# Optimization experiments

Hardware: AMD Instinct MI355X
Metric: run time of the kernel (lower is better)

The kernel has to match this reference:

```python
import jax, jax.numpy as jnp
import numpy as np
from jax import lax

B, S_IN, T_OUT, H, V = 128, 1024, 128, 512, 32


def gru_cell(x, h, Wih, Whh, bih, bhh):
    # PyTorch GRU cell math: gates ordered (r, z, n)
    gi = x @ Wih.T + bih            # (B, 3H)
    gh = h @ Whh.T + bhh            # (B, 3H)
    ir, iz, inn = jnp.split(gi, 3, axis=-1)
    hr, hz, hn = jnp.split(gh, 3, axis=-1)
    r = jax.nn.sigmoid(ir + hr)
    z = jax.nn.sigmoid(iz + hz)
    n = jnp.tanh(inn + r * hn)
    return (1.0 - z) * n + z * h


def setup_inputs() -> dict:
    key = jax.random.key(0)
    ks = jax.random.split(key, 16)
    s = 0.05
    p = lambda k, shape: (jax.random.normal(k, shape, jnp.float32) * s)
    z = lambda n: jnp.zeros((n,), jnp.float32)
    return {
        "x": jax.random.normal(ks[0], (B, S_IN, 2), jnp.float32),
        "embedding": p(ks[1], (V, H)),
        "enc_Wih0": p(ks[2], (3 * H, 2)), "enc_Whh0": p(ks[3], (3 * H, H)),
        "enc_bih0": z(3 * H), "enc_bhh0": z(3 * H),
        "enc_Wih1": p(ks[4], (3 * H, H)), "enc_Whh1": p(ks[5], (3 * H, H)),
        "enc_bih1": z(3 * H), "enc_bhh1": z(3 * H),
        "dec_Wih0": p(ks[6], (3 * H, H)), "dec_Whh0": p(ks[7], (3 * H, H)),
        "dec_bih0": z(3 * H), "dec_bhh0": z(3 * H),
        "dec_Wih1": p(ks[8], (3 * H, H)), "dec_Whh1": p(ks[9], (3 * H, H)),
        "dec_bih1": z(3 * H), "dec_bhh1": z(3 * H),
        "Wq": p(ks[10], (H, H)), "bq": z(H),
        "Wc": p(ks[11], (V, 2 * H)), "bc": z(V),
    }


def reference(x, embedding,
              enc_Wih0, enc_Whh0, enc_bih0, enc_bhh0,
              enc_Wih1, enc_Whh1, enc_bih1, enc_bhh1,
              dec_Wih0, dec_Whh0, dec_bih0, dec_bhh0,
              dec_Wih1, dec_Whh1, dec_bih1, dec_bhh1,
              Wq, bq, Wc, bc):
    b = x.shape[0]
    h_init = jnp.zeros((b, H), x.dtype)

    def run_layer(xs, Wih, Whh, bih, bhh):
        def step(h, xt):
            h2 = gru_cell(xt, h, Wih, Whh, bih, bhh)
            return h2, h2
        return lax.scan(step, h_init, xs)

    # ----- encoder: 2-layer GRU over time -----
    xs = jnp.swapaxes(x, 0, 1)                       # (S, B, 2)
    hT0, ys0 = run_layer(xs, enc_Wih0, enc_Whh0, enc_bih0, enc_bhh0)
    hT1, ys1 = run_layer(ys0, enc_Wih1, enc_Whh1, enc_bih1, enc_bhh1)
    out_enc = jnp.swapaxes(ys1, 0, 1)                # (B, S, H)

    # ----- greedy decoder with Bahdanau-style dot attention -----
    tok0 = jnp.zeros((b,), jnp.int32)                # start token = 0

    def dec_step(carry, _):
        h0, h1, tok = carry
        emb = embedding[tok]                         # (B, H)
        h0n = gru_cell(emb, h0, dec_Wih0, dec_Whh0, dec_bih0, dec_bhh0)
        h1n = gru_cell(h0n, h1, dec_Wih1, dec_Whh1, dec_bih1, dec_bhh1)
        q = h1n @ Wq.T + bq                          # (B, H)
        att = jnp.einsum('bh,bsh->bs', q, out_enc)   # (B, S)
        w = jax.nn.softmax(att, axis=-1)
        ctx = jnp.einsum('bs,bsh->bh', w, out_enc)   # (B, H)
        logits = jnp.concatenate([h1n, ctx], axis=-1) @ Wc.T + bc  # (B, V)
        tok2 = jnp.argmax(logits, axis=-1).astype(jnp.int32)
        return (h0n, h1n, tok2), (logits, w)

    (h0f, h1f, _), (logits_seq, w_seq) = lax.scan(
        dec_step, (hT0, hT1, tok0), None, length=T_OUT)

    vec_out = jnp.swapaxes(logits_seq, 0, 1)         # (B, T_out, V)
    attn_ws = jnp.transpose(w_seq, (1, 2, 0))        # (B, S, T_out)
    hidden = jnp.stack([h0f, h1f], axis=0)           # (n_layers, B, H)
    return vec_out, hidden, attn_ws
```

## Files before the change

kernel.cpp:

```cpp
#include <hip/hip_runtime.h>
#include <hip/hip_fp16.h>
#include <math.h>

#define HH 512
#define BB 128
#define SS 1024
#define TT 128
#define VV 32
#define GG 1536

__device__ __forceinline__ float sigm(float v){ return 1.f/(1.f+expf(-v)); }
__device__ __forceinline__ float fast_tanh(float x){
  float ax = fabsf(x);
  float t = expf(-2.f*ax);
  float r = (1.f - t)/(1.f + t);
  return copysignf(r, x);
}

struct F8 { float v[8]; };

__device__ __forceinline__ F8 load8(const float* p){
  F8 r;
  float4 a = *reinterpret_cast<const float4*>(p);
  float4 b = *reinterpret_cast<const float4*>(p+4);
  r.v[0]=a.x; r.v[1]=a.y; r.v[2]=a.z; r.v[3]=a.w;
  r.v[4]=b.x; r.v[5]=b.y; r.v[6]=b.z; r.v[7]=b.w;
  return r;
}
__device__ __forceinline__ F8 load8(const __half* p){
  F8 r;
  union { float4 f4; __half2 h2[4]; } u;
  u.f4 = *reinterpret_cast<const float4*>(p);
  #pragma unroll
  for (int i=0;i<4;i++){ float2 f = __half22float2(u.h2[i]); r.v[2*i]=f.x; r.v[2*i+1]=f.y; }
  return r;
}
__device__ __forceinline__ void store_enc(float* p, float v){ *p = v; }
__device__ __forceinline__ void store_enc(__half* p, float v){ *p = __float2half(v); }

__global__ void transpose_k(const float* __restrict__ src, float* __restrict__ dst,
                            int R, int C){
  __shared__ float tile[32][33];
  int c0 = blockIdx.x*32, r0 = blockIdx.y*32;
  int tx = threadIdx.x & 31, ty = threadIdx.x >> 5;
  for (int i = ty; i < 32; i += 8){
    int r = r0 + i, c = c0 + tx;
    tile[i][tx] = (r < R && c < C) ? src[(size_t)r*C + c] : 0.f;
  }
  __syncthreads();
  for (int i = ty; i < 32; i += 8){
    int c = c0 + i, r = r0 + tx;
    if (c < C && r < R) dst[(size_t)c*R + r] = tile[tx][i];
  }
}

__global__ void pack_w(const float* __restrict__ src, float* __restrict__ dst, int R){
  int idx = blockIdx.x*256 + threadIdx.x;
  int r = idx >> 9, k = idx & 511;
  dst[((size_t)(k>>2)*R + r)*4 + (k&3)] = src[idx];
}

__device__ __forceinline__ void dot8(const float4* __restrict__ wp, int row, int NR,
                                     const float4* sh4, float acc[8]){
  float4 wc = wp[row];
  for (int kc = 0; kc < 128; kc++) {
    float4 wn = wp[(size_t)(kc+1)*NR + row];
    #pragma unroll
    for (int i = 0; i < 8; i++) {
      float4 h4 = sh4[i*128 + kc];
      acc[i] = fmaf(wc.w, h4.w, fmaf(wc.z, h4.z, fmaf(wc.y, h4.y, fmaf(wc.x, h4.x, acc[i]))));
    }
    wc = wn;
  }
}

template<typename ET>
__global__ __launch_bounds__(192) void enc_step(
    int p,
    const float* __restrict__ x,
    const float* __restrict__ Wih0,
    const float* __restrict__ bih0, const float* __restrict__ bhh0,
    const float* __restrict__ bih1, const float* __restrict__ bhh1,
    const float* __restrict__ Whh0P, const float* __restrict__ Wih1P,
    const float* __restrict__ Whh1P,
    float* __restrict__ gh_all,
    float* __restrict__ h0buf,
    float* __restrict__ h1buf,
    ET* __restrict__ out_enc)
{
  __shared__ float4 sh4[8*128];
  float* shs = (float*)sh4;
  const int bid = blockIdx.x;
  const int xcd = bid & 7, j = bid >> 3;
  const int rc  = xcd*3 + (j % 3);
  const int bch = j / 3;
  const int m   = rc >> 3;
  const int pb  = p & 1;
  if (m == 0 && p >= SS) return;
  if (m >= 1 && p < 1) return;
  const int b0 = bch*8;
  const int tid = threadIdx.x;

  if (m <= 1) {
    float* h0w = h0buf + (size_t)pb*BB*HH;
    for (int idx = tid; idx < 8*HH; idx += 192) {
      int bl = idx >> 9, e = idx & (HH-1);
      int b = b0 + bl;
      float hv;
      if (p == 0) hv = 0.f;
      else {
        int t0 = p - 1;
        float x0v = x[((size_t)b*SS + t0)*2 + 0];
        float x1v = x[((size_t)b*SS + t0)*2 + 1];
        const float* ghp = gh_all + ((size_t)(1-pb)*3 + 0)*BB*GG + (size_t)b*GG;
        float gir = fmaf(x0v, Wih0[e*2],          fmaf(x1v, Wih0[e*2+1],          bih0[e]));
        float giz = fmaf(x0v, Wih0[(HH+e)*2],     fmaf(x1v, Wih0[(HH+e)*2+1],     bih0[HH+e]));
        float gin = fmaf(x0v, Wih0[(2*HH+e)*2],   fmaf(x1v, Wih0[(2*HH+e)*2+1],   bih0[2*HH+e]));
        float ghr = ghp[e]      + bhh0[e];
        float ghz = ghp[HH+e]   + bhh0[HH+e];
        float ghn = ghp[2*HH+e] + bhh0[2*HH+e];
        float hp = (p == 1) ? 0.f : h0buf[(size_t)(1-pb)*BB*HH + (size_t)b*HH + e];
        float r = sigm(gir + ghr);
        float z = sigm(giz + ghz);
        float n = fast_tanh(fmaf(r, ghn, gin));
        hv = (1.f - z)*n + z*hp;
      }
      h0w[(size_t)b*HH + e] = hv;
      shs[idx] = hv;
    }
  } else {
    float* h1w = h1buf + (size_t)pb*BB*HH;
    for (int idx = tid; idx < 8*HH; idx += 192) {
      int bl = idx >> 9, e = idx & (HH-1);
      int b = b0 + bl;
      float hv;
      if (p <= 1) hv = 0.f;
      else {
        const float* gip = gh_all + ((size_t)(1-pb)*3 + 1)*BB*GG + (size_t)b*GG;
        const float* ghp = gh_all + ((size_t)(1-pb)*3 + 2)*BB*GG + (size_t)b*GG;
        float gir = gip[e]      + bih1[e];
        float giz = gip[HH+e]   + bih1[HH+e];
        float gin = gip[2*HH+e] + bih1[2*HH+e];
        float ghr = ghp[e]      + bhh1[e];
        float ghz = ghp[HH+e]   + bhh1[HH+e];
        float ghn = ghp[2*HH+e] + bhh1[2*HH+e];
        float hp = (p == 2) ? 0.f : h1buf[(size_t)(1-pb)*BB*HH + (size_t)b*HH + e];
        float r = sigm(gir + ghr);
        float z = sigm(giz + ghz);
        float n = fast_tanh(fmaf(r, ghn, gin));
        hv = (1.f - z)*n + z*hp;
      }
      h1w[(size_t)b*HH + e] = hv;
      shs[idx] = hv;
      if (p >= 2) store_enc(out_enc + ((size_t)b*SS + (p-2))*HH + e, hv);
    }
  }
  __syncthreads();

  const float4* WP = (const float4*)((m == 0) ? Whh0P : (m == 1) ? Wih1P : Whh1P);
  const int wv = tid >> 6, lane = tid & 63;
  const int row = (rc & 7)*192 + wv*64 + lane;
  float acc[8] = {0,0,0,0,0,0,0,0};
  dot8(WP, row, GG, sh4, acc);
  float* dst = gh_all + ((size_t)pb*3 + m)*BB*GG;
  #pragma unroll
  for (int i = 0; i < 8; i++) dst[(size_t)(b0+i)*GG + row] = acc[i];
}

template<typename ET>
__global__ void enc_bridge(
    const float* __restrict__ gh_all, const float* __restrict__ h1buf,
    const float* __restrict__ bih1, const float* __restrict__ bhh1,
    float* __restrict__ h1init, ET* __restrict__ out_enc)
{
  int idx = blockIdx.x*256 + threadIdx.x;
  int b = idx >> 9, e = idx & (HH-1);
  const float* gip = gh_all + (size_t)1*BB*GG + (size_t)b*GG;
  const float* ghp = gh_all + (size_t)2*BB*GG + (size_t)b*GG;
  float gir = gip[e]      + bih1[e];
  float giz = gip[HH+e]   + bih1[HH+e];
  float gin = gip[2*HH+e] + bih1[2*HH+e];
  float ghr = ghp[e]      + bhh1[e];
  float ghz = ghp[HH+e]   + bhh1[HH+e];
  float ghn = ghp[2*HH+e] + bhh1[2*HH+e];
  float hp = h1buf[(size_t)b*HH + e];
  float r = sigm(gir + ghr);
  float z = sigm(giz + ghz);
  float n = fast_tanh(fmaf(r, ghn, gin));
  float hv = (1.f - z)*n + z*hp;
  h1init[(size_t)b*HH + e] = hv;
  store_enc(out_enc + ((size_t)b*SS + (SS-1))*HH + e, hv);
}

__global__ __launch_bounds__(192) void dec_step1(
    int t,
    const float* __restrict__ embedding,
    const int* __restrict__ tok,
    const float* __restrict__ bih0d, const float* __restrict__ bhh0d,
    const float* __restrict__ Wih0P, const float* __restrict__ Whh0P,
    const float* __restrict__ h0init,
    float* __restrict__ dgh0,
    float* __restrict__ h0d)
{
  __shared__ float4 sh4[8*128];
  float* shs = (float*)sh4;
  const int bid = blockIdx.x;
  const int xcd = bid & 7, j = bid >> 3;
  const int rc  = xcd*2 + (j & 1);
  const int bch = j >> 1;
  const int m   = rc >> 3;
  const int db  = t & 1;
  const int b0 = bch*8;
  const int tid = threadIdx.x;

  if (m == 1) {
    float* hw = h0d + (size_t)db*BB*HH;
    for (int idx = tid; idx < 8*HH; idx += 192) {
      int bl = idx >> 9, e = idx & (HH-1);
      int b = b0 + bl;
      float hv;
      if (t == 0) hv = h0init[(size_t)b*HH + e];
      else {
        const float* gip = dgh0 + ((size_t)(1-db)*2 + 0)*BB*GG + (size_t)b*GG;
        const float* ghp = dgh0 + ((size_t)(1-db)*2 + 1)*BB*GG + (size_t)b*GG;
        float gir = gip[e]      + bih0d[e];
        float giz = gip[HH+e]   + bih0d[HH+e];
        float gin = gip[2*HH+e] + bih0d[2*HH+e];
        float ghr = ghp[e]      + bhh0d[e];
        float ghz = ghp[HH+e]   + bhh0d[HH+e];
        float ghn = ghp[2*HH+e] + bhh0d[2*HH+e];
        float hp = (t == 1) ? h0init[(size_t)b*HH + e]
                            : h0d[(size_t)(1-db)*BB*HH + (size_t)b*HH + e];
        float r = sigm(gir + ghr);
        float z = sigm(giz + ghz);
        float n = fast_tanh(fmaf(r, ghn, gin));
        hv = (1.f - z)*n + z*hp;
      }
      hw[(size_t)b*HH + e] = hv;
      shs[idx] = hv;
    }
  } else {
    for (int idx = tid; idx < 8*HH; idx += 192) {
      int bl = idx >> 9, e = idx & (HH-1);
      int tk = tok[b0 + bl];
      shs[idx] = embedding[(size_t)tk*HH + e];
    }
  }
  __syncthreads();

  const float4* WP = (const float4*)((m == 0) ? Wih0P : Whh0P);
  const int wv = tid >> 6, lane = tid & 63;
  const int row = (rc & 7)*192 + wv*64 + lane;
  float acc[8] = {0,0,0,0,0,0,0,0};
  dot8(WP, row, GG, sh4, acc);
  float* dst = dgh0 + ((size_t)db*2 + m)*BB*GG;
  #pragma unroll
  for (int i = 0; i < 8; i++) dst[(size_t)(b0+i)*GG + row] = acc[i];
}

__global__ __launch_bounds__(192) void dec_step2(
    int t,
    const float* __restrict__ bih0d, const float* __restrict__ bhh0d,
    const float* __restrict__ bih1d, const float* __restrict__ bhh1d,
    const float* __restrict__ Wih1P, const float* __restrict__ Whh1P,
    const float* __restrict__ h1init,
    const float* __restrict__ dgh0,
    const float* __restrict__ h0d,
    float* __restrict__ dgh1,
    float* __restrict__ h1d,
    float* __restrict__ h0n)
{
  __shared__ float4 sh4[8*128];
  float* shs = (float*)sh4;
  const int bid = blockIdx.x;
  const int xcd = bid & 7, j = bid >> 3;
  const int rc  = xcd*2 + (j & 1);
  const int bch = j >> 1;
  const int m   = rc >> 3;
  const int db  = t & 1;
  const int b0 = bch*8;
  const int tid = threadIdx.x;

  if (m == 0) {
    for (int idx = tid; idx < 8*HH; idx += 192) {
      int bl = idx >> 9, e = idx & (HH-1);
      int b = b0 + bl;
      const float* gip = dgh0 + ((size_t)db*2 + 0)*BB*GG + (size_t)b*GG;
      const float* ghp = dgh0 + ((size_t)db*2 + 1)*BB*GG + (size_t)b*GG;
      float gir = gip[e]      + bih0d[e];
      float giz = gip[HH+e]   + bih0d[HH+e];
      float gin = gip[2*HH+e] + bih0d[2*HH+e];
      float ghr = ghp[e]      + bhh0d[e];
      float ghz = ghp[HH+e]   + bhh0d[HH+e];
      float ghn = ghp[2*HH+e] + bhh0d[2*HH+e];
      float hp = h0d[(size_t)db*BB*HH + (size_t)b*HH + e];
      float r = sigm(gir + ghr);
      float z = sigm(giz + ghz);
      float n = fast_tanh(fmaf(r, ghn, gin));
      float hv = (1.f - z)*n + z*hp;
      h0n[(size_t)b*HH + e] = hv;
      shs[idx] = hv;
    }
  } else {
    float* hw = h1d + (size_t)db*BB*HH;
    for (int idx = tid; idx < 8*HH; idx += 192) {
      int bl = idx >> 9, e = idx & (HH-1);
      int b = b0 + bl;
      float hv;
      if (t == 0) hv = h1init[(size_t)b*HH + e];
      else {
        const float* gip = dgh1 + ((size_t)(1-db)*2 + 0)*BB*GG + (size_t)b*GG;
        const float* ghp = dgh1 + ((size_t)(1-db)*2 + 1)*BB*GG + (size_t)b*GG;
        float gir = gip[e]      + bih1d[e];
        float giz = gip[HH+e]   + bih1d[HH+e];
        float gin = gip[2*HH+e] + bih1d[2*HH+e];
        float ghr = ghp[e]      + bhh1d[e];
        float ghz = ghp[HH+e]   + bhh1d[HH+e];
        float ghn = ghp[2*HH+e] + bhh1d[2*HH+e];
        float hp = (t == 1) ? h1init[(size_t)b*HH + e]
                            : h1d[(size_t)(1-db)*BB*HH + (size_t)b*HH + e];
        float r = sigm(gir + ghr);
        float z = sigm(giz + ghz);
        float n = fast_tanh(fmaf(r, ghn, gin));
        hv = (1.f - z)*n + z*hp;
      }
      hw[(size_t)b*HH + e] = hv;
      shs[idx] = hv;
    }
  }
  __syncthreads();

  const float4* WP = (const float4*)((m == 0) ? Wih1P : Whh1P);
  const int wv = tid >> 6, lane = tid & 63;
  const int row = (rc & 7)*192 + wv*64 + lane;
  float acc[8] = {0,0,0,0,0,0,0,0};
  dot8(WP, row, GG, sh4, acc);
  float* dst = dgh1 + ((size_t)db*2 + m)*BB*GG;
  #pragma unroll
  for (int i = 0; i < 8; i++) dst[(size_t)(b0+i)*GG + row] = acc[i];
}

__global__ __launch_bounds__(256) void dec_step3(
    int t,
    const float* __restrict__ bih1d, const float* __restrict__ bhh1d,
    const float* __restrict__ WqP, const float* __restrict__ bq,
    const float* __restrict__ dgh1, const float* __restrict__ h1d,
    float* __restrict__ h1n, float* __restrict__ qbuf)
{
  __shared__ float4 sh4[8*128];
  float* shs = (float*)sh4;
  const int rc = blockIdx.x & 1, bch = blockIdx.x >> 1;
  const int db = t & 1, b0 = bch*8, tid = threadIdx.x;
  for (int idx = tid; idx < 8*HH; idx += 256) {
    int bl = idx >> 9, e = idx & (HH-1);
    int b = b0 + bl;
    const float* gip = dgh1 + ((size_t)db*2 + 0)*BB*GG + (size_t)b*GG;
    const float* ghp = dgh1 + ((size_t)db*2 + 1)*BB*GG + (size_t)b*GG;
    float gir = gip[e]      + bih1d[e];
    float giz = gip[HH+e]   + bih1d[HH+e];
    float gin = gip[2*HH+e] + bih1d[2*HH+e];
    float ghr = ghp[e]      + bhh1d[e];
    float ghz = ghp[HH+e]   + bhh1d[HH+e];
    float ghn = ghp[2*HH+e] + bhh1d[2*HH+e];
    float hp = h1d[(size_t)db*BB*HH + (size_t)b*HH + e];
    float r = sigm(gir + ghr);
    float z = sigm(giz + ghz);
    float n = fast_tanh(fmaf(r, ghn, gin));
    float hv = (1.f - z)*n + z*hp;
    h1n[(size_t)b*HH + e] = hv;
    shs[idx] = hv;
  }
  __syncthreads();
  const int wv = tid >> 6, lane = tid & 63;
  const int row = rc*256 + wv*64 + lane;
  float acc[8] = {0,0,0,0,0,0,0,0};
  dot8((const float4*)WqP, row, HH, sh4, acc);
  #pragma unroll
  for (int i = 0; i < 8; i++) qbuf[(size_t)(b0+i)*HH + row] = acc[i] + bq[row];
}

template<typename ET>
__global__ __launch_bounds__(256) void dec_attn(
    const float* __restrict__ qbuf, const ET* __restrict__ out_enc,
    float* __restrict__ att, float* __restrict__ pm, float* __restrict__ pl,
    float* __restrict__ pctx)
{
  const int b = blockIdx.x >> 3, sc = blockIdx.x & 7;
  const int tid = threadIdx.x, wv = tid >> 6, lane = tid & 63;
  const F8 q = load8(qbuf + (size_t)b*HH + lane*8);
  const ET* encb = out_enc + (size_t)b*SS*HH;
  float mrun = -1e30f, lrun = 0.f;
  float c[8] = {0,0,0,0,0,0,0,0};
  float attkeep = 0.f;
  const int sbase = sc*128 + wv*32;
  for (int ii = 0; ii < 32; ii++) {
    const F8 e = load8(encb + (size_t)(sbase + ii)*HH + lane*8);
    float d = 0.f;
    #pragma unroll
    for (int j = 0; j < 8; j++) d = fmaf(q.v[j], e.v[j], d);
    #pragma unroll
    for (int off = 32; off >= 1; off >>= 1) d += __shfl_xor(d, off, 64);
    if (lane == ii) attkeep = d;
    float mnew = fmaxf(mrun, d);
    float scal = expf(mrun - mnew);
    float pv = expf(d - mnew);
    lrun = fmaf(lrun, scal, pv);
    #pragma unroll
    for (int j = 0; j < 8; j++) c[j] = fmaf(c[j], scal, pv*e.v[j]);
    mrun = mnew;
  }
  if (lane < 32) att[(size_t)b*SS + sbase + lane] = attkeep;
  __shared__ float lm[4], ll[4];
  __shared__ float lctx[4][HH];
  if (lane == 0) { lm[wv] = mrun; ll[wv] = lrun; }
  #pragma unroll
  for (int j = 0; j < 8; j++) lctx[wv][lane*8+j] = c[j];
  __syncthreads();
  float mb = fmaxf(fmaxf(lm[0],lm[1]), fmaxf(lm[2],lm[3]));
  float e0w = expf(lm[0]-mb), e1w = expf(lm[1]-mb), e2w = expf(lm[2]-mb), e3w = expf(lm[3]-mb);
  if (tid == 0) {
    pm[b*8+sc] = mb;
    pl[b*8+sc] = e0w*ll[0] + e1w*ll[1] + e2w*ll[2] + e3w*ll[3];
  }
  for (int k2 = tid; k2 < HH; k2 += 256) {
    float s = e0w*lctx[0][k2] + e1w*lctx[1][k2] + e2w*lctx[2][k2] + e3w*lctx[3][k2];
    pctx[((size_t)b*8 + sc)*HH + k2] = s;
  }
}

__global__ __launch_bounds__(256) void dec_final(
    int t,
    const float* __restrict__ pm, const float* __restrict__ pl,
    const float* __restrict__ pctx, const float* __restrict__ att,
    const float* __restrict__ h1n,
    const float* __restrict__ WcT, const float* __restrict__ bc,
    float* __restrict__ out_vec, float* __restrict__ out_attn,
    int* __restrict__ tok)
{
  const int b = blockIdx.x, tid = threadIdx.x;
  __shared__ float s_hc[2*HH];
  __shared__ float s_red[8][33];
  float pmv[8], plv[8];
  #pragma unroll
  for (int c = 0; c < 8; c++){ pmv[c] = pm[b*8+c]; plv[c] = pl[b*8+c]; }
  float mg = pmv[0];
  #pragma unroll
  for (int c = 1; c < 8; c++) mg = fmaxf(mg, pmv[c]);
  float epm[8]; float lg = 0.f;
  #pragma unroll
  for (int c = 0; c < 8; c++){ epm[c] = expf(pmv[c]-mg); lg += epm[c]*plv[c]; }
  float inv_lg = 1.f/lg;
  for (int k = tid; k < HH; k += 256) {
    float s = 0.f;
    #pragma unroll
    for (int c = 0; c < 8; c++) s += epm[c]*pctx[((size_t)b*8+c)*HH + k];
    s_hc[HH + k] = s * inv_lg;
    s_hc[k] = h1n[(size_t)b*HH + k];
  }
  __syncthreads();
  for (int s = tid; s < SS; s += 256)
    out_attn[((size_t)b*SS + s)*TT + t] = expf(att[(size_t)b*SS + s] - mg) * inv_lg;
  const int v = tid & 31, part = tid >> 5;
  float pacc = 0.f;
  for (int k = part*128; k < part*128 + 128; k++)
    pacc = fmaf(s_hc[k], WcT[(size_t)k*VV + v], pacc);
  s_red[part][v] = pacc;
  __syncthreads();
  if (tid < 32) {
    float lv = bc[tid];
    #pragma unroll
    for (int c = 0; c < 8; c++) lv += s_red[c][tid];
    out_vec[((size_t)b*TT + t)*VV + tid] = lv;
    float bv = lv; int bi = tid;
    #pragma unroll
    for (int off = 16; off >= 1; off >>= 1) {
      float ov = __shfl_xor(bv, off, 64);
      int   oi = __shfl_xor(bi, off, 64);
      if (ov > bv || (ov == bv && oi < bi)) { bv = ov; bi = oi; }
    }
    if (tid == 0) tok[b] = bi;
  }
}

struct Bufs {
  const float *x, *emb;
  const float *eWih0, *ebih0, *ebhh0, *ebih1, *ebhh1;
  const float *dbih0, *dbhh0, *dbih1, *dbhh1, *bq, *bc;
  float *gh_all, *dgh0, *dgh1;
  float *h0buf, *h1buf, *h0d, *h1d, *h0n, *h1n, *h1init, *qbuf;
  float *att, *pmb, *plb, *pctx;
  int   *tok;
  float *Whh0P, *Wih1P, *Whh1P, *dWih0P, *dWhh0P, *dWih1P, *dWhh1P, *WqP, *WcT;
  float *out_vec, *out_hid, *out_attn;
};

template<typename ET>
static void run_pipeline(const Bufs& B, ET* out_enc, hipStream_t stream) {
  hipMemsetAsync(B.tok, 0, BB*sizeof(int), stream);
  for (int p = 0; p <= SS; p++)
    enc_step<ET><<<dim3(384), dim3(192), 0, stream>>>(p,
        B.x, B.eWih0, B.ebih0, B.ebhh0, B.ebih1, B.ebhh1,
        B.Whh0P, B.Wih1P, B.Whh1P,
        B.gh_all, B.h0buf, B.h1buf, out_enc);
  enc_bridge<ET><<<dim3(256), dim3(256), 0, stream>>>(
      B.gh_all, B.h1buf, B.ebih1, B.ebhh1, B.h1init, out_enc);
  const float* h0init = B.h0buf;

  for (int t = 0; t < TT; t++) {
    dec_step1<<<dim3(256), dim3(192), 0, stream>>>(t,
        B.emb, B.tok, B.dbih0, B.dbhh0, B.dWih0P, B.dWhh0P, h0init, B.dgh0, B.h0d);
    dec_step2<<<dim3(256), dim3(192), 0, stream>>>(t,
        B.dbih0, B.dbhh0, B.dbih1, B.dbhh1, B.dWih1P, B.dWhh1P, B.h1init,
        B.dgh0, B.h0d, B.dgh1, B.h1d, B.h0n);
    dec_step3<<<dim3(32), dim3(256), 0, stream>>>(t,
        B.dbih1, B.dbhh1, B.WqP, B.bq, B.dgh1, B.h1d, B.h1n, B.qbuf);
    dec_attn<ET><<<dim3(1024), dim3(256), 0, stream>>>(
        B.qbuf, out_enc, B.att, B.pmb, B.plb, B.pctx);
    dec_final<<<dim3(128), dim3(256), 0, stream>>>(t,
        B.pmb, B.plb, B.pctx, B.att, B.h1n, B.WcT, B.bc,
        B.out_vec, B.out_attn, B.tok);
  }
  hipMemcpyAsync(B.out_hid, B.h0n, (size_t)BB*HH*sizeof(float),
                 hipMemcpyDeviceToDevice, stream);
  hipMemcpyAsync(B.out_hid + (size_t)BB*HH, B.h1n, (size_t)BB*HH*sizeof(float),
                 hipMemcpyDeviceToDevice, stream);
}

extern "C" void kernel_launch(void* const* d_in, const int* in_sizes, int n_in,
                              void* d_out, int out_size, void* d_ws, size_t ws_size,
                              hipStream_t stream) {
  const float* x      = (const float*)d_in[0];
  const float* emb    = (const float*)d_in[1];
  const float* eWih0  = (const float*)d_in[2];
  const float* eWhh0  = (const float*)d_in[3];
  const float* ebih0  = (const float*)d_in[4];
  const float* ebhh0  = (const float*)d_in[5];
  const float* eWih1  = (const float*)d_in[6];
  const float* eWhh1  = (const float*)d_in[7];
  const float* ebih1  = (const float*)d_in[8];
  const float* ebhh1  = (const float*)d_in[9];
  const float* dWih0  = (const float*)d_in[10];
  const float* dWhh0  = (const float*)d_in[11];
  const float* dbih0  = (const float*)d_in[12];
  const float* dbhh0  = (const float*)d_in[13];
  const float* dWih1  = (const float*)d_in[14];
  const float* dWhh1  = (const float*)d_in[15];
  const float* dbih1  = (const float*)d_in[16];
  const float* dbhh1  = (const float*)d_in[17];
  const float* Wq     = (const float*)d_in[18];
  const float* bq     = (const float*)d_in[19];
  const float* Wc     = (const float*)d_in[20];
  const float* bc     = (const float*)d_in[21];
  (void)in_sizes; (void)n_in; (void)out_size;

  float* ws = (float*)d_ws;
  size_t off = 0;
  auto alloc = [&](size_t n){ float* p = ws + off; off += n; return p; };
  const size_t PKB = (size_t)GG*HH + 4*GG;
  const size_t PKQ = (size_t)HH*HH + 4*HH;

  Bufs B;
  B.x = x; B.emb = emb;
  B.eWih0 = eWih0; B.ebih0 = ebih0; B.ebhh0 = ebhh0; B.ebih1 = ebih1; B.ebhh1 = ebhh1;
  B.dbih0 = dbih0; B.dbhh0 = dbhh0; B.dbih1 = dbih1; B.dbhh1 = dbhh1;
  B.bq = bq; B.bc = bc;

  B.gh_all  = alloc((size_t)2*3*BB*GG);
  B.dgh0    = alloc((size_t)2*2*BB*GG);
  B.dgh1    = alloc((size_t)2*2*BB*GG);
  B.h0buf   = alloc((size_t)2*BB*HH);
  B.h1buf   = alloc((size_t)2*BB*HH);
  B.h0d     = alloc((size_t)2*BB*HH);
  B.h1d     = alloc((size_t)2*BB*HH);
  B.h0n     = alloc((size_t)BB*HH);
  B.h1n     = alloc((size_t)BB*HH);
  B.h1init  = alloc((size_t)BB*HH);
  B.qbuf    = alloc((size_t)BB*HH);
  B.att     = alloc((size_t)BB*SS);
  B.pmb     = alloc((size_t)BB*8);
  B.plb     = alloc((size_t)BB*8);
  B.pctx    = alloc((size_t)BB*8*HH);
  B.tok     = (int*)alloc((size_t)BB);
  B.Whh0P   = alloc(PKB);
  B.Wih1P   = alloc(PKB);
  B.Whh1P   = alloc(PKB);
  B.dWih0P  = alloc(PKB);
  B.dWhh0P  = alloc(PKB);
  B.dWih1P  = alloc(PKB);
  B.dWhh1P  = alloc(PKB);
  B.WqP     = alloc(PKQ);
  B.WcT     = alloc((size_t)2*HH*VV);

  B.out_vec  = (float*)d_out;
  B.out_hid  = (float*)d_out + (size_t)BB*TT*VV;
  B.out_attn = (float*)d_out + (size_t)BB*TT*VV + (size_t)2*BB*HH;

  dim3 tb(256);
  pack_w<<<dim3(GG*HH/256), tb, 0, stream>>>(eWhh0, B.Whh0P, GG);
  pack_w<<<dim3(GG*HH/256), tb, 0, stream>>>(eWih1, B.Wih1P, GG);
  pack_w<<<dim3(GG*HH/256), tb, 0, stream>>>(eWhh1, B.Whh1P, GG);
  pack_w<<<dim3(GG*HH/256), tb, 0, stream>>>(dWih0, B.dWih0P, GG);
  pack_w<<<dim3(GG*HH/256), tb, 0, stream>>>(dWhh0, B.dWhh0P, GG);
  pack_w<<<dim3(GG*HH/256), tb, 0, stream>>>(dWih1, B.dWih1P, GG);
  pack_w<<<dim3(GG*HH/256), tb, 0, stream>>>(dWhh1, B.dWhh1P, GG);
  pack_w<<<dim3(HH*HH/256), tb, 0, stream>>>(Wq, B.WqP, HH);
  transpose_k<<<dim3(32,1),  tb, 0, stream>>>(Wc, B.WcT, VV, 2*HH);

  const size_t enc_elems = (size_t)BB*SS*HH;
  const size_t need32 = (off + enc_elems) * sizeof(float);
  if (ws_size >= need32) {
    float* out_enc = ws + off;
    run_pipeline<float>(B, out_enc, stream);
  } else {
    __half* out_enc = reinterpret_cast<__half*>(ws + off);
    run_pipeline<__half>(B, out_enc, stream);
  }
}
```

Measured before the change: 97.19 ms.

## Replace per-step kernel launches with persistent cooperative kernels using grid barriers

```diff
diff --git a/kernel.cpp b/kernel.cpp
--- a/kernel.cpp
+++ b/kernel.cpp
@@ -8,6 +8,9 @@
 #define TT 128
 #define VV 32
 #define GG 1536
+
+#define ENC_BLOCKS 384
+#define DEC_BLOCKS 256
 
 __device__ __forceinline__ float sigm(float v){ return 1.f/(1.f+expf(-v)); }
 __device__ __forceinline__ float fast_tanh(float x){
@@ -37,6 +40,18 @@
 }
 __device__ __forceinline__ void store_enc(float* p, float v){ *p = v; }
 __device__ __forceinline__ void store_enc(__half* p, float v){ *p = __float2half(v); }
+
+__device__ __forceinline__ void grid_bar(unsigned* bar, unsigned target){
+  __syncthreads();
+  if (threadIdx.x == 0) {
+    __threadfence();
+    atomicAdd(bar, 1u);
+    while (__hip_atomic_load(bar, __ATOMIC_RELAXED, __HIP_MEMORY_SCOPE_AGENT) < target)
+      __builtin_amdgcn_s_sleep(1);
+    __threadfence();
+  }
+  __syncthreads();
+}
 
 __global__ void transpose_k(const float* __restrict__ src, float* __restrict__ dst,
                             int R, int C){
@@ -74,97 +89,99 @@
   }
 }
 
+struct EncArgs {
+  const float *x, *Wih0, *bih0, *bhh0, *bih1, *bhh1;
+  const float *Whh0P, *Wih1P, *Whh1P;
+  float *gh_all, *h0buf, *h1buf;
+  void *out_enc;
+  unsigned *bar;
+};
+
 template<typename ET>
-__global__ __launch_bounds__(192) void enc_step(
-    int p,
-    const float* __restrict__ x,
-    const float* __restrict__ Wih0,
-    const float* __restrict__ bih0, const float* __restrict__ bhh0,
-    const float* __restrict__ bih1, const float* __restrict__ bhh1,
-    const float* __restrict__ Whh0P, const float* __restrict__ Wih1P,
-    const float* __restrict__ Whh1P,
-    float* __restrict__ gh_all,
-    float* __restrict__ h0buf,
-    float* __restrict__ h1buf,
-    ET* __restrict__ out_enc)
+__global__ __launch_bounds__(192) void enc_persist(EncArgs A)
 {
-  __shared__ float4 sh4[8*128];
+  __shared__ float4 sh4[1024];
   float* shs = (float*)sh4;
   const int bid = blockIdx.x;
   const int xcd = bid & 7, j = bid >> 3;
   const int rc  = xcd*3 + (j % 3);
   const int bch = j / 3;
   const int m   = rc >> 3;
-  const int pb  = p & 1;
-  if (m == 0 && p >= SS) return;
-  if (m >= 1 && p < 1) return;
-  const int b0 = bch*8;
+  const int b0  = bch*8;
   const int tid = threadIdx.x;
-
-  if (m <= 1) {
-    float* h0w = h0buf + (size_t)pb*BB*HH;
-    for (int idx = tid; idx < 8*HH; idx += 192) {
-      int bl = idx >> 9, e = idx & (HH-1);
-      int b = b0 + bl;
-      float hv;
-      if (p == 0) hv = 0.f;
-      else {
-        int t0 = p - 1;
-        float x0v = x[((size_t)b*SS + t0)*2 + 0];
-        float x1v = x[((size_t)b*SS + t0)*2 + 1];
-        const float* ghp = gh_all + ((size_t)(1-pb)*3 + 0)*BB*GG + (size_t)b*GG;
-        float gir = fmaf(x0v, Wih0[e*2],          fmaf(x1v, Wih0[e*2+1],          bih0[e]));
-        float giz = fmaf(x0v, Wih0[(HH+e)*2],     fmaf(x1v, Wih0[(HH+e)*2+1],     bih0[HH+e]));
-        float gin = fmaf(x0v, Wih0[(2*HH+e)*2],   fmaf(x1v, Wih0[(2*HH+e)*2+1],   bih0[2*HH+e]));
-        float ghr = ghp[e]      + bhh0[e];
-        float ghz = ghp[HH+e]   + bhh0[HH+e];
-        float ghn = ghp[2*HH+e] + bhh0[2*HH+e];
-        float hp = (p == 1) ? 0.f : h0buf[(size_t)(1-pb)*BB*HH + (size_t)b*HH + e];
-        float r = sigm(gir + ghr);
-        float z = sigm(giz + ghz);
-        float n = fast_tanh(fmaf(r, ghn, gin));
-        hv = (1.f - z)*n + z*hp;
-      }
-      h0w[(size_t)b*HH + e] = hv;
-      shs[idx] = hv;
-    }
-  } else {
-    float* h1w = h1buf + (size_t)pb*BB*HH;
-    for (int idx = tid; idx < 8*HH; idx += 192) {
-      int bl = idx >> 9, e = idx & (HH-1);
-      int b = b0 + bl;
-      float hv;
-      if (p <= 1) hv = 0.f;
-      else {
-        const float* gip = gh_all + ((size_t)(1-pb)*3 + 1)*BB*GG + (size_t)b*GG;
-        const float* ghp = gh_all + ((size_t)(1-pb)*3 + 2)*BB*GG + (size_t)b*GG;
-        float gir = gip[e]      + bih1[e];
-        float giz = gip[HH+e]   + bih1[HH+e];
-        float gin = gip[2*HH+e] + bih1[2*HH+e];
-        float ghr = ghp[e]      + bhh1[e];
-        float ghz = ghp[HH+e]   + bhh1[HH+e];
-        float ghn = ghp[2*HH+e] + bhh1[2*HH+e];
-        float hp = (p == 2) ? 0.f : h1buf[(size_t)(1-pb)*BB*HH + (size_t)b*HH + e];
-        float r = sigm(gir + ghr);
-        float z = sigm(giz + ghz);
-        float n = fast_tanh(fmaf(r, ghn, gin));
-        hv = (1.f - z)*n + z*hp;
-      }
-      h1w[(size_t)b*HH + e] = hv;
-      shs[idx] = hv;
-      if (p >= 2) store_enc(out_enc + ((size_t)b*SS + (p-2))*HH + e, hv);
-    }
-  }
-  __syncthreads();
-
-  const float4* WP = (const float4*)((m == 0) ? Whh0P : (m == 1) ? Wih1P : Whh1P);
-  const int wv = tid >> 6, lane = tid & 63;
-  const int row = (rc & 7)*192 + wv*64 + lane;
-  float acc[8] = {0,0,0,0,0,0,0,0};
-  dot8(WP, row, GG, sh4, acc);
-  float* dst = gh_all + ((size_t)pb*3 + m)*BB*GG;
-  #pragma unroll
-  for (int i = 0; i < 8; i++) dst[(size_t)(b0+i)*GG + row] = acc[i];
+  ET* out_enc = (ET*)A.out_enc;
+
+  for (int p = 0; p <= SS; ++p) {
+    const int pb = p & 1;
+    const bool active = !((m == 0 && p >= SS) || (m >= 1 && p < 1));
+    if (active) {
+      if (m <= 1) {
+        float* h0w = A.h0buf + (size_t)pb*BB*HH;
+        for (int idx = tid; idx < 8*HH; idx += 192) {
+          int bl = idx >> 9, e = idx & (HH-1);
+          int b = b0 + bl;
+          float hv;
+          if (p == 0) hv = 0.f;
+          else {
+            int t0 = p - 1;
+            float x0v = A.x[((size_t)b*SS + t0)*2 + 0];
+            float x1v = A.x[((size_t)b*SS + t0)*2 + 1];
+            const float* ghp = A.gh_all + ((size_t)(1-pb)*3 + 0)*BB*GG + (size_t)b*GG;
+            float gir = fmaf(x0v, A.Wih0[e*2],        fmaf(x1v, A.Wih0[e*2+1],        A.bih0[e]));
+            float giz = fmaf(x0v, A.Wih0[(HH+e)*2],   fmaf(x1v, A.Wih0[(HH+e)*2+1],   A.bih0[HH+e]));
+            float gin = fmaf(x0v, A.Wih0[(2*HH+e)*2], fmaf(x1v, A.Wih0[(2*HH+e)*2+1], A.bih0[2*HH+e]));
+            float ghr = ghp[e]      + A.bhh0[e];
+            float ghz = ghp[HH+e]   + A.bhh0[HH+e];
+            float ghn = ghp[2*HH+e] + A.bhh0[2*HH+e];
+            float hp = (p == 1) ? 0.f : A.h0buf[(size_t)(1-pb)*BB*HH + (size_t)b*HH + e];
+            float r = sigm(gir + ghr);
+            float z = sigm(giz + ghz);
+            float n = fast_tanh(fmaf(r, ghn, gin));
+            hv = (1.f - z)*n + z*hp;
+          }
+          h0w[(size_t)b*HH + e] = hv;
+          shs[idx] = hv;
+        }
+      } else {
+        float* h1w = A.h1buf + (size_t)pb*BB*HH;
+        for (int idx = tid; idx < 8*HH; idx += 192) {
+          int bl = idx >> 9, e = idx & (HH-1);
+          int b = b0 + bl;
+          float hv;
+          if (p <= 1) hv = 0.f;
+          else {
+            const float* gip = A.gh_all + ((size_t)(1-pb)*3 + 1)*BB*GG + (size_t)b*GG;
+            const float* ghp = A.gh_all + ((size_t)(1-pb)*3 + 2)*BB*GG + (size_t)b*GG;
+            float gir = gip[e]      + A.bih1[e];
+            float giz = gip[HH+e]   + A.bih1[HH+e];
+            float gin = gip[2*HH+e] + A.bih1[2*HH+e];
+            float ghr = ghp[e]      + A.bhh1[e];
+            float ghz = ghp[HH+e]   + A.bhh1[HH+e];
+            float ghn = ghp[2*HH+e] + A.bhh1[2*HH+e];
+            float hp = (p == 2) ? 0.f : A.h1buf[(size_t)(1-pb)*BB*HH + (size_t)b*HH + e];
+            float r = sigm(gir + ghr);
+            float z = sigm(giz + ghz);
+            float n = fast_tanh(fmaf(r, ghn, gin));
+            hv = (1.f - z)*n + z*hp;
+          }
+          h1w[(size_t)b*HH + e] = hv;
+          shs[idx] = hv;
+          if (p >= 2) store_enc(out_enc + ((size_t)b*SS + (p-2))*HH + e, hv);
+        }
+      }
+      __syncthreads();
+
+      const float4* WP = (const float4*)((m == 0) ? A.Whh0P : (m == 1) ? A.Wih1P : A.Whh1P);
+      const int wv = tid >> 6, lane = tid & 63;
+      const int row = (rc & 7)*192 + wv*64 + lane;
+      float acc[8] = {0,0,0,0,0,0,0,0};
+      dot8(WP, row, GG, sh4, acc);
+      float* dst = A.gh_all + ((size_t)pb*3 + m)*BB*GG;
+      #pragma unroll
+      for (int i = 0; i < 8; i++) dst[(size_t)(b0+i)*GG + row] = acc[i];
+    }
+    grid_bar(A.bar, (unsigned)(p+1) * (unsigned)ENC_BLOCKS);
+  }
 }
 
 template<typename ET>
@@ -192,338 +209,276 @@
   store_enc(out_enc + ((size_t)b*SS + (SS-1))*HH + e, hv);
 }
 
-__global__ __launch_bounds__(192) void dec_step1(
-    int t,
-    const float* __restrict__ embedding,
-    const int* __restrict__ tok,
-    const float* __restrict__ bih0d, const float* __restrict__ bhh0d,
-    const float* __restrict__ Wih0P, const float* __restrict__ Whh0P,
-    const float* __restrict__ h0init,
-    float* __restrict__ dgh0,
-    float* __restrict__ h0d)
+struct DecArgs {
+  const float *emb;
+  const float *bih0d, *bhh0d, *bih1d, *bhh1d, *bq, *bc;
+  const float *Wih0P, *Whh0P, *Wih1P, *Whh1P, *WqP, *WcT;
+  const float *h0init, *h1init;
+  float *dgh0, *dgh1, *h0d, *h1d, *h0n, *h1n, *qbuf;
+  float *att, *pm, *pl, *pctx;
+  int *tok;
+  void *out_enc;
+  float *out_vec, *out_attn, *out_hid;
+  unsigned *bar;
+};
+
+template<typename ET>
+__global__ __launch_bounds__(256) void dec_persist(DecArgs A)
 {
-  __shared__ float4 sh4[8*128];
-  float* shs = (float*)sh4;
+  __shared__ float4 smem4[1024];
+  float* smem = (float*)smem4;
+  __shared__ float lm[4], ll[4];
+  __shared__ float s_red[8][33];
   const int bid = blockIdx.x;
-  const int xcd = bid & 7, j = bid >> 3;
-  const int rc  = xcd*2 + (j & 1);
-  const int bch = j >> 1;
-  const int m   = rc >> 3;
-  const int db  = t & 1;
-  const int b0 = bch*8;
   const int tid = threadIdx.x;
-
-  if (m == 1) {
-    float* hw = h0d + (size_t)db*BB*HH;
-    for (int idx = tid; idx < 8*HH; idx += 192) {
-      int bl = idx >> 9, e = idx & (HH-1);
-      int b = b0 + bl;
-      float hv;
-      if (t == 0) hv = h0init[(size_t)b*HH + e];
-      else {
-        const float* gip = dgh0 + ((size_t)(1-db)*2 + 0)*BB*GG + (size_t)b*GG;
-        const float* ghp = dgh0 + ((size_t)(1-db)*2 + 1)*BB*GG + (size_t)b*GG;
-        float gir = gip[e]      + bih0d[e];
-        float giz = gip[HH+e]   + bih0d[HH+e];
-        float gin = gip[2*HH+e] + bih0d[2*HH+e];
-        float ghr = ghp[e]      + bhh0d[e];
-        float ghz = ghp[HH+e]   + bhh0d[HH+e];
-        float ghn = ghp[2*HH+e] + bhh0d[2*HH+e];
-        float hp = (t == 1) ? h0init[(size_t)b*HH + e]
-                            : h0d[(size_t)(1-db)*BB*HH + (size_t)b*HH + e];
+  const int wv = tid >> 6, lane = tid & 63;
+  ET* out_enc = (ET*)A.out_enc;
+  unsigned gens = 0;
+
+  for (int t = 0; t < TT; ++t) {
+    const int db = t & 1;
+
+    if (bid < 192) {
+      const int m = bid / 96, v = bid % 96, rowu = v / 16, bch = v % 16, b0 = bch*8;
+      if (m == 1) {
+        for (int idx = tid; idx < 8*HH; idx += 256) {
+          int bl = idx >> 9, e = idx & (HH-1);
+          int b = b0 + bl;
+          float hv;
+          if (t == 0) hv = A.h0init[(size_t)b*HH + e];
+          else {
+            const float* gip = A.dgh0 + ((size_t)(1-db)*2 + 0)*BB*GG + (size_t)b*GG;
+            const float* ghp = A.dgh0 + ((size_t)(1-db)*2 + 1)*BB*GG + (size_t)b*GG;
+            float gir = gip[e]      + A.bih0d[e];
+            float giz = gip[HH+e]   + A.bih0d[HH+e];
+            float gin = gip[2*HH+e] + A.bih0d[2*HH+e];
+            float ghr = ghp[e]      + A.bhh0d[e];
+            float ghz = ghp[HH+e]   + A.bhh0d[HH+e];
+            float ghn = ghp[2*HH+e] + A.bhh0d[2*HH+e];
+            float hp = (t == 1) ? A.h0init[(size_t)b*HH + e]
+                                : A.h0d[(size_t)(1-db)*BB*HH + (size_t)b*HH + e];
+            float r = sigm(gir + ghr);
+            float z = sigm(giz + ghz);
+            float n = fast_tanh(fmaf(r, ghn, gin));
+            hv = (1.f - z)*n + z*hp;
+          }
+          smem[idx] = hv;
+          if (rowu == 0) A.h0d[(size_t)db*BB*HH + (size_t)b*HH + e] = hv;
+        }
+      } else {
+        for (int idx = tid; idx < 8*HH; idx += 256) {
+          int bl = idx >> 9, e = idx & (HH-1);
+          int tk = A.tok[b0 + bl];
+          smem[idx] = A.emb[(size_t)tk*HH + e];
+        }
+      }
+      __syncthreads();
+      const float4* WP = (const float4*)((m == 0) ? A.Wih0P : A.Whh0P);
+      const int row = rowu*256 + tid;
+      float acc[8] = {0,0,0,0,0,0,0,0};
+      dot8(WP, row, GG, smem4, acc);
+      float* dst = A.dgh0 + ((size_t)db*2 + m)*BB*GG;
+      #pragma unroll
+      for (int i = 0; i < 8; i++) dst[(size_t)(b0+i)*GG + row] = acc[i];
+    }
+    grid_bar(A.bar, (++gens) * (unsigned)DEC_BLOCKS);
+
+    if (bid < 192) {
+      const int m = bid / 96, v = bid % 96, rowu = v / 16, bch = v % 16, b0 = bch*8;
+      if (m == 0) {
+        for (int idx = tid; idx < 8*HH; idx += 256) {
+          int bl = idx >> 9, e = idx & (HH-1);
+          int b = b0 + bl;
+          const float* gip = A.dgh0 + ((size_t)db*2 + 0)*BB*GG + (size_t)b*GG;
+          const float* ghp = A.dgh0 + ((size_t)db*2 + 1)*BB*GG + (size_t)b*GG;
+          float gir = gip[e]      + A.bih0d[e];
+          float giz = gip[HH+e]   + A.bih0d[HH+e];
+          float gin = gip[2*HH+e] + A.bih0d[2*HH+e];
+          float ghr = ghp[e]      + A.bhh0d[e];
+          float ghz = ghp[HH+e]   + A.bhh0d[HH+e];
+          float ghn = ghp[2*HH+e] + A.bhh0d[2*HH+e];
+          float hp = A.h0d[(size_t)db*BB*HH + (size_t)b*HH + e];
+          float r = sigm(gir + ghr);
+          float z = sigm(giz + ghz);
+          float n = fast_tanh(fmaf(r, ghn, gin));
+          float hv = (1.f - z)*n + z*hp;
+          smem[idx] = hv;
+          if (rowu == 0) A.h0n[(size_t)b*HH + e] = hv;
+        }
+      } else {
+        for (int idx = tid; idx < 8*HH; idx += 256) {
+          int bl = idx >> 9, e = idx & (HH-1);
+          int b = b0 + bl;
+          float hv;
+          if (t == 0) hv = A.h1init[(size_t)b*HH + e];
+          else {
+            const float* gip = A.dgh1 + ((size_t)(1-db)*2 + 0)*BB*GG + (size_t)b*GG;
+            const float* ghp = A.dgh1 + ((size_t)(1-db)*2 + 1)*BB*GG + (size_t)b*GG;
+            float gir = gip[e]      + A.bih1d[e];
+            float giz = gip[HH+e]   + A.bih1d[HH+e];
+            float gin = gip[2*HH+e] + A.bih1d[2*HH+e];
+            float ghr = ghp[e]      + A.bhh1d[e];
+            float ghz = ghp[HH+e]   + A.bhh1d[HH+e];
+            float ghn = ghp[2*HH+e] + A.bhh1d[2*HH+e];
+            float hp = (t == 1) ? A.h1init[(size_t)b*HH + e]
+                                : A.h1d[(size_t)(1-db)*BB*HH + (size_t)b*HH + e];
+            float r = sigm(gir + ghr);
+            float z = sigm(giz + ghz);
+            float n = fast_tanh(fmaf(r, ghn, gin));
+            hv = (1.f - z)*n + z*hp;
+          }
+          smem[idx] = hv;
+          if (rowu == 0) A.h1d[(size_t)db*BB*HH + (size_t)b*HH + e] = hv;
+        }
+      }
+      __syncthreads();
+      const float4* WP = (const float4*)((m == 0) ? A.Wih1P : A.Whh1P);
+      const int row = rowu*256 + tid;
+      float acc[8] = {0,0,0,0,0,0,0,0};
+      dot8(WP, row, GG, smem4, acc);
+      float* dst = A.dgh1 + ((size_t)db*2 + m)*BB*GG;
+      #pragma unroll
+      for (int i = 0; i < 8; i++) dst[(size_t)(b0+i)*GG + row] = acc[i];
+    }
+    grid_bar(A.bar, (++gens) * (unsigned)DEC_BLOCKS);
+
+    if (bid < 32) {
+      const int rowu = bid & 1, bch = bid >> 1, b0 = bch*8;
+      for (int idx = tid; idx < 8*HH; idx += 256) {
+        int bl = idx >> 9, e = idx & (HH-1);
+        int b = b0 + bl;
+        const float* gip = A.dgh1 + ((size_t)db*2 + 0)*BB*GG + (size_t)b*GG;
+        const float* ghp = A.dgh1 + ((size_t)db*2 + 1)*BB*GG + (size_t)b*GG;
+        float gir = gip[e]      + A.bih1d[e];
+        float giz = gip[HH+e]   + A.bih1d[HH+e];
+        float gin = gip[2*HH+e] + A.bih1d[2*HH+e];
+        float ghr = ghp[e]      + A.bhh1d[e];
+        float ghz = ghp[HH+e]   + A.bhh1d[HH+e];
+        float ghn = ghp[2*HH+e] + A.bhh1d[2*HH+e];
+        float hp = A.h1d[(size_t)db*BB*HH + (size_t)b*HH + e];
         float r = sigm(gir + ghr);
         float z = sigm(giz + ghz);
         float n = fast_tanh(fmaf(r, ghn, gin));
-        hv = (1.f - z)*n + z*hp;
-      }
-      hw[(size_t)b*HH + e] = hv;
-      shs[idx] = hv;
-    }
-  } else {
-    for (int idx = tid; idx < 8*HH; idx += 192) {
-      int bl = idx >> 9, e = idx & (HH-1);
-      int tk = tok[b0 + bl];
-      shs[idx] = embedding[(size_t)tk*HH + e];
-    }
-  }
-  __syncthreads();
-
-  const float4* WP = (const float4*)((m == 0) ? Wih0P : Whh0P);
-  const int wv = tid >> 6, lane = tid & 63;
-  const int row = (rc & 7)*192 + wv*64 + lane;
-  float acc[8] = {0,0,0,0,0,0,0,0};
-  dot8(WP, row, GG, sh4, acc);
-  float* dst = dgh0 + ((size_t)db*2 + m)*BB*GG;
-  #pragma unroll
-  for (int i = 0; i < 8; i++) dst[(size_t)(b0+i)*GG + row] = acc[i];
-}
-
-__global__ __launch_bounds__(192) void dec_step2(
-    int t,
-    const float* __restrict__ bih0d, const float* __restrict__ bhh0d,
-    const float* __restrict__ bih1d, const float* __restrict__ bhh1d,
-    const float* __restrict__ Wih1P, const float* __restrict__ Whh1P,
-    const float* __restrict__ h1init,
-    const float* __restrict__ dgh0,
-    const float* __restrict__ h0d,
-    float* __restrict__ dgh1,
-    float* __restrict__ h1d,
-    float* __restrict__ h0n)
-{
-  __shared__ float4 sh4[8*128];
-  float* shs = (float*)sh4;
-  const int bid = blockIdx.x;
-  const int xcd = bid & 7, j = bid >> 3;
-  const int rc  = xcd*2 + (j & 1);
-  const int bch = j >> 1;
-  const int m   = rc >> 3;
-  const int db  = t & 1;
-  const int b0 = bch*8;
-  const int tid = threadIdx.x;
-
-  if (m == 0) {
-    for (int idx = tid; idx < 8*HH; idx += 192) {
-      int bl = idx >> 9, e = idx & (HH-1);
-      int b = b0 + bl;
-      const float* gip = dgh0 + ((size_t)db*2 + 0)*BB*GG + (size_t)b*GG;
-      const float* ghp = dgh0 + ((size_t)db*2 + 1)*BB*GG + (size_t)b*GG;
-      float gir = gip[e]      + bih0d[e];
-      float giz = gip[HH+e]   + bih0d[HH+e];
-      float gin = gip[2*HH+e] + bih0d[2*HH+e];
-      float ghr = ghp[e]      + bhh0d[e];
-      float ghz = ghp[HH+e]   + bhh0d[HH+e];
-      float ghn = ghp[2*HH+e] + bhh0d[2*HH+e];
-      float hp = h0d[(size_t)db*BB*HH + (size_t)b*HH + e];
-      float r = sigm(gir + ghr);
-      float z = sigm(giz + ghz);
-      float n = fast_tanh(fmaf(r, ghn, gin));
-      float hv = (1.f - z)*n + z*hp;
-      h0n[(size_t)b*HH + e] = hv;
-      shs[idx] = hv;
-    }
-  } else {
-    float* hw = h1d + (size_t)db*BB*HH;
-    for (int idx = tid; idx < 8*HH; idx += 192) {
-      int bl = idx >> 9, e = idx & (HH-1);
-      int b = b0 + bl;
-      float hv;
-      if (t == 0) hv = h1init[(size_t)b*HH + e];
-      else {
-        const float* gip = dgh1 + ((size_t)(1-db)*2 + 0)*BB*GG + (size_t)b*GG;
-        const float* ghp = dgh1 + ((size_t)(1-db)*2 + 1)*BB*GG + (size_t)b*GG;
-        float gir = gip[e]      + bih1d[e];
-        float giz = gip[HH+e]   + bih1d[HH+e];
-        float gin = gip[2*HH+e] + bih1d[2*HH+e];
-        float ghr = ghp[e]      + bhh1d[e];
-        float ghz = ghp[HH+e]   + bhh1d[HH+e];
-        float ghn = ghp[2*HH+e] + bhh1d[2*HH+e];
-        float hp = (t == 1) ? h1init[(size_t)b*HH + e]
-                            : h1d[(size_t)(1-db)*BB*HH + (size_t)b*HH + e];
-        float r = sigm(gir + ghr);
-        float z = sigm(giz + ghz);
-        float n = fast_tanh(fmaf(r, ghn, gin));
-        hv = (1.f - z)*n + z*hp;
-      }
-      hw[(size_t)b*HH + e] = hv;
-      shs[idx] = hv;
-    }
-  }
-  __syncthreads();
-
-  const float4* WP = (const float4*)((m == 0) ? Wih1P : Whh1P);
-  const int wv = tid >> 6, lane = tid & 63;
-  const int row = (rc & 7)*192 + wv*64 + lane;
-  float acc[8] = {0,0,0,0,0,0,0,0};
-  dot8(WP, row, GG, sh4, acc);
-  float* dst = dgh1 + ((size_t)db*2 + m)*BB*GG;
-  #pragma unroll
-  for (int i = 0; i < 8; i++) dst[(size_t)(b0+i)*GG + row] = acc[i];
-}
-
-__global__ __launch_bounds__(256) void dec_step3(
-    int t,
-    const float* __restrict__ bih1d, const float* __restrict__ bhh1d,
-    const float* __restrict__ WqP, const float* __restrict__ bq,
-    const float* __restrict__ dgh1, const float* __restrict__ h1d,
-    float* __restrict__ h1n, float* __restrict__ qbuf)
-{
-  __shared__ float4 sh4[8*128];
-  float* shs = (float*)sh4;
-  const int rc = blockIdx.x & 1, bch = blockIdx.x >> 1;
-  const int db = t & 1, b0 = bch*8, tid = threadIdx.x;
-  for (int idx = tid; idx < 8*HH; idx += 256) {
-    int bl = idx >> 9, e = idx & (HH-1);
-    int b = b0 + bl;
-    const float* gip = dgh1 + ((size_t)db*2 + 0)*BB*GG + (size_t)b*GG;
-    const float* ghp = dgh1 + ((size_t)db*2 + 1)*BB*GG + (size_t)b*GG;
-    float gir = gip[e]      + bih1d[e];
-    float giz = gip[HH+e]   + bih1d[HH+e];
-    float gin = gip[2*HH+e] + bih1d[2*HH+e];
-    float ghr = ghp[e]      + bhh1d[e];
-    float ghz = ghp[HH+e]   + bhh1d[HH+e];
-    float ghn = ghp[2*HH+e] + bhh1d[2*HH+e];
-    float hp = h1d[(size_t)db*BB*HH + (size_t)b*HH + e];
-    float r = sigm(gir + ghr);
-    float z = sigm(giz + ghz);
-    float n = fast_tanh(fmaf(r, ghn, gin));
-    float hv = (1.f - z)*n + z*hp;
-    h1n[(size_t)b*HH + e] = hv;
-    shs[idx] = hv;
-  }
-  __syncthreads();
-  const int wv = tid >> 6, lane = tid & 63;
-  const int row = rc*256 + wv*64 + lane;
-  float acc[8] = {0,0,0,0,0,0,0,0};
-  dot8((const float4*)WqP, row, HH, sh4, acc);
-  #pragma unroll
-  for (int i = 0; i < 8; i++) qbuf[(size_t)(b0+i)*HH + row] = acc[i] + bq[row];
+        float hv = (1.f - z)*n + z*hp;
+        smem[idx] = hv;
+        if (rowu == 0) A.h1n[(size_t)b*HH + e] = hv;
+      }
+      __syncthreads();
+      const int row = rowu*256 + tid;
+      float acc[8] = {0,0,0,0,0,0,0,0};
+      dot8((const float4*)A.WqP, row, HH, smem4, acc);
+      #pragma unroll
+      for (int i = 0; i < 8; i++) A.qbuf[(size_t)(b0+i)*HH + row] = acc[i] + A.bq[row];
+    }
+    grid_bar(A.bar, (++gens) * (unsigned)DEC_BLOCKS);
+
+    for (int u = bid; u < BB*8; u += DEC_BLOCKS) {
+      const int b = u >> 3, sc = u & 7;
+      __syncthreads();
+      const F8 q = load8(A.qbuf + (size_t)b*HH + lane*8);
+      const ET* encb = out_enc + (size_t)b*SS*HH;
+      float mrun = -1e30f, lrun = 0.f;
+      float c[8] = {0,0,0,0,0,0,0,0};
+      float attkeep = 0.f;
+      const int sbase = sc*128 + wv*32;
+      for (int ii = 0; ii < 32; ii++) {
+        const F8 e = load8(encb + (size_t)(sbase + ii)*HH + lane*8);
+        float d = 0.f;
+        #pragma unroll
+        for (int jj = 0; jj < 8; jj++) d = fmaf(q.v[jj], e.v[jj], d);
+        #pragma unroll
+        for (int off = 32; off >= 1; off >>= 1) d += __shfl_xor(d, off, 64);
+        if (lane == ii) attkeep = d;
+        float mnew = fmaxf(mrun, d);
+        float scal = expf(mrun - mnew);
+        float pv = expf(d - mnew);
+        lrun = fmaf(lrun, scal, pv);
+        #pragma unroll
+        for (int jj = 0; jj < 8; jj++) c[jj] = fmaf(c[jj], scal, pv*e.v[jj]);
+        mrun = mnew;
+      }
+      if (lane < 32) A.att[(size_t)b*SS + sbase + lane] = attkeep;
+      if (lane == 0) { lm[wv] = mrun; ll[wv] = lrun; }
+      #pragma unroll
+      for (int jj = 0; jj < 8; jj++) smem[wv*HH + lane*8 + jj] = c[jj];
+      __syncthreads();
+      float mb = fmaxf(fmaxf(lm[0],lm[1]), fmaxf(lm[2],lm[3]));
+      float e0w = expf(lm[0]-mb), e1w = expf(lm[1]-mb), e2w = expf(lm[2]-mb), e3w = expf(lm[3]-mb);
+      if (tid == 0) {
+        A.pm[b*8+sc] = mb;
+        A.pl[b*8+sc] = e0w*ll[0] + e1w*ll[1] + e2w*ll[2] + e3w*ll[3];
+      }
+      for (int k2 = tid; k2 < HH; k2 += 256) {
+        float s = e0w*smem[0*HH+k2] + e1w*smem[1*HH+k2] + e2w*smem[2*HH+k2] + e3w*smem[3*HH+k2];
+        A.pctx[((size_t)b*8 + sc)*HH + k2] = s;
+      }
+    }
+    grid_bar(A.bar, (++gens) * (unsigned)DEC_BLOCKS);
+
+    if (bid < BB) {
+      const int b = bid;
+      float* s_hc = smem;
+      float pmv[8], plv[8];
+      #pragma unroll
+      for (int c8 = 0; c8 < 8; c8++){ pmv[c8] = A.pm[b*8+c8]; plv[c8] = A.pl[b*8+c8]; }
+      float mg = pmv[0];
+      #pragma unroll
+      for (int c8 = 1; c8 < 8; c8++) mg = fmaxf(mg, pmv[c8]);
+      float epm[8]; float lg = 0.f;
+      #pragma unroll
+      for (int c8 = 0; c8 < 8; c8++){ epm[c8] = expf(pmv[c8]-mg); lg += epm[c8]*plv[c8]; }
+      float inv_lg = 1.f/lg;
+      for (int k = tid; k < HH; k += 256) {
+        float s = 0.f;
+        #pragma unroll
+        for (int c8 = 0; c8 < 8; c8++) s += epm[c8]*A.pctx[((size_t)b*8+c8)*HH + k];
+        s_hc[HH + k] = s * inv_lg;
+        s_hc[k] = A.h1n[(size_t)b*HH + k];
+      }
+      __syncthreads();
+      for (int s = tid; s < SS; s += 256)
+        A.out_attn[((size_t)b*SS + s)*TT + t] = expf(A.att[(size_t)b*SS + s] - mg) * inv_lg;
+      const int v = tid & 31, part = tid >> 5;
+      float pacc = 0.f;
+      for (int k = part*128; k < part*128 + 128; k++)
+        pacc = fmaf(s_hc[k], A.WcT[(size_t)k*VV + v], pacc);
+      s_red[part][v] = pacc;
+      __syncthreads();
+      if (tid < 32) {
+        float lv = A.bc[tid];
+        #pragma unroll
+        for (int c8 = 0; c8 < 8; c8++) lv += s_red[c8][tid];
+        A.out_vec[((size_t)b*TT + t)*VV + tid] = lv;
+        float bv = lv; int bi = tid;
+        #pragma unroll
+        for (int off = 16; off >= 1; off >>= 1) {
+          float ov = __shfl_xor(bv, off, 64);
+          int   oi = __shfl_xor(bi, off, 64);
+          if (ov > bv || (ov == bv && oi < bi)) { bv = ov; bi = oi; }
+        }
+        if (tid == 0) A.tok[b] = bi;
+      }
+    }
+    grid_bar(A.bar, (++gens) * (unsigned)DEC_BLOCKS);
+  }
+
+  for (int i = bid*256 + tid; i < BB*HH; i += DEC_BLOCKS*256) {
+    A.out_hid[i] = A.h0n[i];
+    A.out_hid[BB*HH + i] = A.h1n[i];
+  }
 }
 
 template<typename ET>
-__global__ __launch_bounds__(256) void dec_attn(
-    const float* __restrict__ qbuf, const ET* __restrict__ out_enc,
-    float* __restrict__ att, float* __restrict__ pm, float* __restrict__ pl,
-    float* __restrict__ pctx)
-{
-  const int b = blockIdx.x >> 3, sc = blockIdx.x & 7;
-  const int tid = threadIdx.x, wv = tid >> 6, lane = tid & 63;
-  const F8 q = load8(qbuf + (size_t)b*HH + lane*8);
-  const ET* encb = out_enc + (size_t)b*SS*HH;
-  float mrun = -1e30f, lrun = 0.f;
-  float c[8] = {0,0,0,0,0,0,0,0};
-  float attkeep = 0.f;
-  const int sbase = sc*128 + wv*32;
-  for (int ii = 0; ii < 32; ii++) {
-    const F8 e = load8(encb + (size_t)(sbase + ii)*HH + lane*8);
-    float d = 0.f;
-    #pragma unroll
-    for (int j = 0; j < 8; j++) d = fmaf(q.v[j], e.v[j], d);
-    #pragma unroll
-    for (int off = 32; off >= 1; off >>= 1) d += __shfl_xor(d, off, 64);
-    if (lane == ii) attkeep = d;
-    float mnew = fmaxf(mrun, d);
-    float scal = expf(mrun - mnew);
-    float pv = expf(d - mnew);
-    lrun = fmaf(lrun, scal, pv);
-    #pragma unroll
-    for (int j = 0; j < 8; j++) c[j] = fmaf(c[j], scal, pv*e.v[j]);
-    mrun = mnew;
-  }
-  if (lane < 32) att[(size_t)b*SS + sbase + lane] = attkeep;
-  __shared__ float lm[4], ll[4];
-  __shared__ float lctx[4][HH];
-  if (lane == 0) { lm[wv] = mrun; ll[wv] = lrun; }
-  #pragma unroll
-  for (int j = 0; j < 8; j++) lctx[wv][lane*8+j] = c[j];
-  __syncthreads();
-  float mb = fmaxf(fmaxf(lm[0],lm[1]), fmaxf(lm[2],lm[3]));
-  float e0w = expf(lm[0]-mb), e1w = expf(lm[1]-mb), e2w = expf(lm[2]-mb), e3w = expf(lm[3]-mb);
-  if (tid == 0) {
-    pm[b*8+sc] = mb;
-    pl[b*8+sc] = e0w*ll[0] + e1w*ll[1] + e2w*ll[2] + e3w*ll[3];
-  }
-  for (int k2 = tid; k2 < HH; k2 += 256) {
-    float s = e0w*lctx[0][k2] + e1w*lctx[1][k2] + e2w*lctx[2][k2] + e3w*lctx[3][k2];
-    pctx[((size_t)b*8 + sc)*HH + k2] = s;
-  }
-}
-
-__global__ __launch_bounds__(256) void dec_final(
-    int t,
-    const float* __restrict__ pm, const float* __restrict__ pl,
-    const float* __restrict__ pctx, const float* __restrict__ att,
-    const float* __restrict__ h1n,
-    const float* __restrict__ WcT, const float* __restrict__ bc,
-    float* __restrict__ out_vec, float* __restrict__ out_attn,
-    int* __restrict__ tok)
-{
-  const int b = blockIdx.x, tid = threadIdx.x;
-  __shared__ float s_hc[2*HH];
-  __shared__ float s_red[8][33];
-  float pmv[8], plv[8];
-  #pragma unroll
-  for (int c = 0; c < 8; c++){ pmv[c] = pm[b*8+c]; plv[c] = pl[b*8+c]; }
-  float mg = pmv[0];
-  #pragma unroll
-  for (int c = 1; c < 8; c++) mg = fmaxf(mg, pmv[c]);
-  float epm[8]; float lg = 0.f;
-  #pragma unroll
-  for (int c = 0; c < 8; c++){ epm[c] = expf(pmv[c]-mg); lg += epm[c]*plv[c]; }
-  float inv_lg = 1.f/lg;
-  for (int k = tid; k < HH; k += 256) {
-    float s = 0.f;
-    #pragma unroll
-    for (int c = 0; c < 8; c++) s += epm[c]*pctx[((size_t)b*8+c)*HH + k];
-    s_hc[HH + k] = s * inv_lg;
-    s_hc[k] = h1n[(size_t)b*HH + k];
-  }
-  __syncthreads();
-  for (int s = tid; s < SS; s += 256)
-    out_attn[((size_t)b*SS + s)*TT + t] = expf(att[(size_t)b*SS + s] - mg) * inv_lg;
-  const int v = tid & 31, part = tid >> 5;
-  float pacc = 0.f;
-  for (int k = part*128; k < part*128 + 128; k++)
-    pacc = fmaf(s_hc[k], WcT[(size_t)k*VV + v], pacc);
-  s_red[part][v] = pacc;
-  __syncthreads();
-  if (tid < 32) {
-    float lv = bc[tid];
-    #pragma unroll
-    for (int c = 0; c < 8; c++) lv += s_red[c][tid];
-    out_vec[((size_t)b*TT + t)*VV + tid] = lv;
-    float bv = lv; int bi = tid;
-    #pragma unroll
-    for (int off = 16; off >= 1; off >>= 1) {
-      float ov = __shfl_xor(bv, off, 64);
-      int   oi = __shfl_xor(bi, off, 64);
-      if (ov > bv || (ov == bv && oi < bi)) { bv = ov; bi = oi; }
-    }
-    if (tid == 0) tok[b] = bi;
-  }
-}
-
-struct Bufs {
-  const float *x, *emb;
-  const float *eWih0, *ebih0, *ebhh0, *ebih1, *ebhh1;
-  const float *dbih0, *dbhh0, *dbih1, *dbhh1, *bq, *bc;
-  float *gh_all, *dgh0, *dgh1;
-  float *h0buf, *h1buf, *h0d, *h1d, *h0n, *h1n, *h1init, *qbuf;
-  float *att, *pmb, *plb, *pctx;
-  int   *tok;
-  float *Whh0P, *Wih1P, *Whh1P, *dWih0P, *dWhh0P, *dWih1P, *dWhh1P, *WqP, *WcT;
-  float *out_vec, *out_hid, *out_attn;
-};
-
-template<typename ET>
-static void run_pipeline(const Bufs& B, ET* out_enc, hipStream_t stream) {
-  hipMemsetAsync(B.tok, 0, BB*sizeof(int), stream);
-  for (int p = 0; p <= SS; p++)
-    enc_step<ET><<<dim3(384), dim3(192), 0, stream>>>(p,
-        B.x, B.eWih0, B.ebih0, B.ebhh0, B.ebih1, B.ebhh1,
-        B.Whh0P, B.Wih1P, B.Whh1P,
-        B.gh_all, B.h0buf, B.h1buf, out_enc);
+static void launch_all(EncArgs& EA, DecArgs& DA, hipStream_t stream) {
+  void* ep[1] = { &EA };
+  hipLaunchCooperativeKernel((const void*)&enc_persist<ET>, dim3(ENC_BLOCKS), dim3(192),
+                             ep, 0, stream);
   enc_bridge<ET><<<dim3(256), dim3(256), 0, stream>>>(
-      B.gh_all, B.h1buf, B.ebih1, B.ebhh1, B.h1init, out_enc);
-  const float* h0init = B.h0buf;
-
-  for (int t = 0; t < TT; t++) {
-    dec_step1<<<dim3(256), dim3(192), 0, stream>>>(t,
-        B.emb, B.tok, B.dbih0, B.dbhh0, B.dWih0P, B.dWhh0P, h0init, B.dgh0, B.h0d);
-    dec_step2<<<dim3(256), dim3(192), 0, stream>>>(t,
-        B.dbih0, B.dbhh0, B.dbih1, B.dbhh1, B.dWih1P, B.dWhh1P, B.h1init,
-        B.dgh0, B.h0d, B.dgh1, B.h1d, B.h0n);
-    dec_step3<<<dim3(32), dim3(256), 0, stream>>>(t,
-        B.dbih1, B.dbhh1, B.WqP, B.bq, B.dgh1, B.h1d, B.h1n, B.qbuf);
-    dec_attn<ET><<<dim3(1024), dim3(256), 0, stream>>>(
-        B.qbuf, out_enc, B.att, B.pmb, B.plb, B.pctx);
-    dec_final<<<dim3(128), dim3(256), 0, stream>>>(t,
-        B.pmb, B.plb, B.pctx, B.att, B.h1n, B.WcT, B.bc,
-        B.out_vec, B.out_attn, B.tok);
-  }
-  hipMemcpyAsync(B.out_hid, B.h0n, (size_t)BB*HH*sizeof(float),
-                 hipMemcpyDeviceToDevice, stream);
-  hipMemcpyAsync(B.out_hid + (size_t)BB*HH, B.h1n, (size_t)BB*HH*sizeof(float),
-                 hipMemcpyDeviceToDevice, stream);
+      EA.gh_all, EA.h1buf, EA.bih1, EA.bhh1,
+      (float*)DA.h1init, (ET*)EA.out_enc);
+  void* dp[1] = { &DA };
+  hipLaunchCooperativeKernel((const void*)&dec_persist<ET>, dim3(DEC_BLOCKS), dim3(256),
+                             dp, 0, stream);
 }
 
 extern "C" void kernel_launch(void* const* d_in, const int* in_sizes, int n_in,
@@ -559,60 +514,82 @@
   const size_t PKB = (size_t)GG*HH + 4*GG;
   const size_t PKQ = (size_t)HH*HH + 4*HH;
 
-  Bufs B;
-  B.x = x; B.emb = emb;
-  B.eWih0 = eWih0; B.ebih0 = ebih0; B.ebhh0 = ebhh0; B.ebih1 = ebih1; B.ebhh1 = ebhh1;
-  B.dbih0 = dbih0; B.dbhh0 = dbhh0; B.dbih1 = dbih1; B.dbhh1 = dbhh1;
-  B.bq = bq; B.bc = bc;
-
-  B.gh_all  = alloc((size_t)2*3*BB*GG);
-  B.dgh0    = alloc((size_t)2*2*BB*GG);
-  B.dgh1    = alloc((size_t)2*2*BB*GG);
-  B.h0buf   = alloc((size_t)2*BB*HH);
-  B.h1buf   = alloc((size_t)2*BB*HH);
-  B.h0d     = alloc((size_t)2*BB*HH);
-  B.h1d     = alloc((size_t)2*BB*HH);
-  B.h0n     = alloc((size_t)BB*HH);
-  B.h1n     = alloc((size_t)BB*HH);
-  B.h1init  = alloc((size_t)BB*HH);
-  B.qbuf    = alloc((size_t)BB*HH);
-  B.att     = alloc((size_t)BB*SS);
-  B.pmb     = alloc((size_t)BB*8);
-  B.plb     = alloc((size_t)BB*8);
-  B.pctx    = alloc((size_t)BB*8*HH);
-  B.tok     = (int*)alloc((size_t)BB);
-  B.Whh0P   = alloc(PKB);
-  B.Wih1P   = alloc(PKB);
-  B.Whh1P   = alloc(PKB);
-  B.dWih0P  = alloc(PKB);
-  B.dWhh0P  = alloc(PKB);
-  B.dWih1P  = alloc(PKB);
-  B.dWhh1P  = alloc(PKB);
-  B.WqP     = alloc(PKQ);
-  B.WcT     = alloc((size_t)2*HH*VV);
-
-  B.out_vec  = (float*)d_out;
-  B.out_hid  = (float*)d_out + (size_t)BB*TT*VV;
-  B.out_attn = (float*)d_out + (size_t)BB*TT*VV + (size_t)2*BB*HH;
+  float* gh_all  = alloc((size_t)2*3*BB*GG);
+  float* dgh0    = alloc((size_t)2*2*BB*GG);
+  float* dgh1    = alloc((size_t)2*2*BB*GG);
+  float* h0buf   = alloc((size_t)2*BB*HH);
+  float* h1buf   = alloc((size_t)2*BB*HH);
+  float* h0d     = alloc((size_t)2*BB*HH);
+  float* h1d     = alloc((size_t)2*BB*HH);
+  float* h0n     = alloc((size_t)BB*HH);
+  float* h1n     = alloc((size_t)BB*HH);
+  float* h1init  = alloc((size_t)BB*HH);
+  float* qbuf    = alloc((size_t)BB*HH);
+  float* att     = alloc((size_t)BB*SS);
+  float* pmb     = alloc((size_t)BB*8);
+  float* plb     = alloc((size_t)BB*8);
+  float* pctx    = alloc((size_t)BB*8*HH);
+  int*   tok     = (int*)alloc((size_t)BB);
+  float* barbuf  = alloc((size_t)64);
+  float* Whh0P   = alloc(PKB);
+  float* Wih1P   = alloc(PKB);
+  float* Whh1P   = alloc(PKB);
+  float* dWih0P  = alloc(PKB);
+  float* dWhh0P  = alloc(PKB);
+  float* dWih1P  = alloc(PKB);
+  float* dWhh1P  = alloc(PKB);
+  float* WqP     = alloc(PKQ);
+  float* WcT     = alloc((size_t)2*HH*VV);
+
+  float* out_vec  = (float*)d_out;
+  float* out_hid  = (float*)d_out + (size_t)BB*TT*VV;
+  float* out_attn = (float*)d_out + (size_t)BB*TT*VV + (size_t)2*BB*HH;
+
+  hipMemsetAsync(barbuf, 0, 64*sizeof(float), stream);
+  hipMemsetAsync(tok, 0, BB*sizeof(int), stream);
 
   dim3 tb(256);
-  pack_w<<<dim3(GG*HH/256), tb, 0, stream>>>(eWhh0, B.Whh0P, GG);
-  pack_w<<<dim3(GG*HH/256), tb, 0, stream>>>(eWih1, B.Wih1P, GG);
-  pack_w<<<dim3(GG*HH/256), tb, 0, stream>>>(eWhh1, B.Whh1P, GG);
-  pack_w<<<dim3(GG*HH/256), tb, 0, stream>>>(dWih0, B.dWih0P, GG);
-  pack_w<<<dim3(GG*HH/256), tb, 0, stream>>>(dWhh0, B.dWhh0P, GG);
-  pack_w<<<dim3(GG*HH/256), tb, 0, stream>>>(dWih1, B.dWih1P, GG);
-  pack_w<<<dim3(GG*HH/256), tb, 0, stream>>>(dWhh1, B.dWhh1P, GG);
-  pack_w<<<dim3(HH*HH/256), tb, 0, stream>>>(Wq, B.WqP, HH);
-  transpose_k<<<dim3(32,1),  tb, 0, stream>>>(Wc, B.WcT, VV, 2*HH);
+  pack_w<<<dim3(GG*HH/256), tb, 0, stream>>>(eWhh0, Whh0P, GG);
+  pack_w<<<dim3(GG*HH/256), tb, 0, stream>>>(eWih1, Wih1P, GG);
+  pack_w<<<dim3(GG*HH/256), tb, 0, stream>>>(eWhh1, Whh1P, GG);
+  pack_w<<<dim3(GG*HH/256), tb, 0, stream>>>(dWih0, dWih0P, GG);
+  pack_w<<<dim3(GG*HH/256), tb, 0, stream>>>(dWhh0, dWhh0P, GG);
+  pack_w<<<dim3(GG*HH/256), tb, 0, stream>>>(dWih1, dWih1P, GG);
+  pack_w<<<dim3(GG*HH/256), tb, 0, stream>>>(dWhh1, dWhh1P, GG);
+  pack_w<<<dim3(HH*HH/256), tb, 0, stream>>>(Wq, WqP, HH);
+  transpose_k<<<dim3(32,1),  tb, 0, stream>>>(Wc, WcT, VV, 2*HH);
+
+  EncArgs EA;
+  EA.x = x; EA.Wih0 = eWih0; EA.bih0 = ebih0; EA.bhh0 = ebhh0;
+  EA.bih1 = ebih1; EA.bhh1 = ebhh1;
+  EA.Whh0P = Whh0P; EA.Wih1P = Wih1P; EA.Whh1P = Whh1P;
+  EA.gh_all = gh_all; EA.h0buf = h0buf; EA.h1buf = h1buf;
+  EA.bar = (unsigned*)barbuf;
+
+  DecArgs DA;
+  DA.emb = emb;
+  DA.bih0d = dbih0; DA.bhh0d = dbhh0; DA.bih1d = dbih1; DA.bhh1d = dbhh1;
+  DA.bq = bq; DA.bc = bc;
+  DA.Wih0P = dWih0P; DA.Whh0P = dWhh0P; DA.Wih1P = dWih1P; DA.Whh1P = dWhh1P;
+  DA.WqP = WqP; DA.WcT = WcT;
+  DA.h0init = h0buf;
+  DA.h1init = h1init;
+  DA.dgh0 = dgh0; DA.dgh1 = dgh1; DA.h0d = h0d; DA.h1d = h1d;
+  DA.h0n = h0n; DA.h1n = h1n; DA.qbuf = qbuf;
+  DA.att = att; DA.pm = pmb; DA.pl = plb; DA.pctx = pctx;
+  DA.tok = tok;
+  DA.out_vec = out_vec; DA.out_attn = out_attn; DA.out_hid = out_hid;
+  DA.bar = (unsigned*)(barbuf + 32);
 
   const size_t enc_elems = (size_t)BB*SS*HH;
   const size_t need32 = (off + enc_elems) * sizeof(float);
   if (ws_size >= need32) {
     float* out_enc = ws + off;
-    run_pipeline<float>(B, out_enc, stream);
+    EA.out_enc = out_enc; DA.out_enc = out_enc;
+    launch_all<float>(EA, DA, stream);
   } else {
     __half* out_enc = reinterpret_cast<__half*>(ws + off);
-    run_pipeline<__half>(B, out_enc, stream);
-  }
-}
+    EA.out_enc = out_enc; DA.out_enc = out_enc;
+    launch_all<__half>(EA, DA, stream);
+  }
+}
```

Result: slower. 126.4 ms (+30.1%).
